# Optimization experiments

Measured on AMD Instinct MI355X. Metric: run time of the kernel, lower is better.

The kernel has to match this reference:

```python
import jax, jax.numpy as jnp
import numpy as np

# ViT-Base-ish encoder: 256x256 img, patch 8 -> N=1024 tokens, dim 768, 8 layers
B, C, H, W = 8, 3, 256, 256
P, D, DEPTH, HEADS, DH, MLP = 8, 768, 8, 12, 64, 3072
N = (H // P) * (W // P)
INNER = HEADS * DH  # 768
EPS = 1e-5


def setup_inputs() -> dict:
    key = jax.random.key(0)
    ks = jax.random.split(key, 8)
    s = lambda i, shape, scale=0.02: jax.random.normal(ks[i], shape, jnp.float32) * scale
    return {
        "x": s(0, (B, C, H, W), 1.0),
        "w_conv": s(1, (D, C, P, P)),          # OIHW conv kernel (patch embed)
        "b_conv": jnp.zeros((D,), jnp.float32),
        "pos_emb": s(2, (1, N, D)),
        "ln1_w": jnp.ones((DEPTH, D), jnp.float32),
        "ln1_b": jnp.zeros((DEPTH, D), jnp.float32),
        "qkv_w": s(3, (DEPTH, D, 3 * INNER)),  # stored [in,out]; Linear has no bias
        "out_w": s(4, (DEPTH, INNER, D)),
        "out_b": jnp.zeros((DEPTH, D), jnp.float32),
        "ln2_w": jnp.ones((DEPTH, D), jnp.float32),
        "ln2_b": jnp.zeros((DEPTH, D), jnp.float32),
        "w1": s(5, (DEPTH, D, MLP)),
        "b1": jnp.zeros((DEPTH, MLP), jnp.float32),
        "w2": s(6, (DEPTH, MLP, D)),
        "b2": jnp.zeros((DEPTH, D), jnp.float32),
    }


def _layernorm(x, w, b):
    m = jnp.mean(x, axis=-1, keepdims=True)
    v = jnp.mean(jnp.square(x - m), axis=-1, keepdims=True)
    return (x - m) * jax.lax.rsqrt(v + EPS) * w + b


def _encoder(x, w_conv, b_conv, pos_emb, ln1_w, ln1_b, qkv_w, out_w, out_b,
             ln2_w, ln2_b, w1, b1, w2, b2):
    # PatchEmbed: strided conv -> flatten(2).transpose(1,2)
    h = jax.lax.conv_general_dilated(
        x, w_conv, window_strides=(P, P), padding='VALID',
        dimension_numbers=('NCHW', 'OIHW', 'NCHW'))
    h = h + b_conv[None, :, None, None]
    h = h.reshape(B, D, N).transpose(0, 2, 1)  # [B, N, D]
    h = h + pos_emb
    scale = DH ** -0.5

    def block(h, p):
        l1w, l1b, qkvw, ow, ob, l2w, l2b, W1, B1, W2, B2 = p
        # PreNorm + MHSA
        y = _layernorm(h, l1w, l1b)
        qkv = y @ qkvw                                   # [B,N,3*INNER]
        q, k, v = jnp.split(qkv, 3, axis=-1)
        split_heads = lambda t: t.reshape(B, N, HEADS, DH).transpose(0, 2, 1, 3)
        q, k, v = split_heads(q), split_heads(k), split_heads(v)
        attn = jax.nn.softmax(jnp.einsum('bhnd,bhmd->bhnm', q, k) * scale, axis=-1)
        o = jnp.einsum('bhnm,bhmd->bhnd', attn, v)
        o = o.transpose(0, 2, 1, 3).reshape(B, N, INNER)
        h = h + (o @ ow + ob)
        # PreNorm + FFN (exact GELU, dropout=0)
        y = _layernorm(h, l2w, l2b)
        h = h + (jax.nn.gelu(y @ W1 + B1, approximate=False) @ W2 + B2)
        return h, None

    h, _ = jax.lax.scan(block, h, (ln1_w, ln1_b, qkv_w, out_w, out_b,
                                   ln2_w, ln2_b, w1, b1, w2, b2))
    return h


def reference(x, w_conv, b_conv, pos_emb, ln1_w, ln1_b, qkv_w, out_w, out_b,
              ln2_w, ln2_b, w1, b1, w2, b2):
    return _encoder(x, w_conv, b_conv, pos_emb, ln1_w, ln1_b, qkv_w, out_w,
                    out_b, ln2_w, ln2_b, w1, b1, w2, b2)
```

## Files before the change

kernel.cpp:

```cpp
#include <hip/hip_runtime.h>
#include <math.h>

#define BATCH 8
#define CIN 3
#define HIMG 256
#define WIMG 256
#define PATCH 8
#define DMODEL 768
#define DEPTH 8
#define HEADS 12
#define DHEAD 64
#define MLPDIM 3072
#define NTOK 1024
#define INNER 768
#define MROWS (BATCH * NTOK)
#define QKVS (3 * INNER)
#define KPATCH (CIN * PATCH * PATCH)
#define LNEPS 1e-5f
#define QSCALE 0.18033688011112042f

typedef __attribute__((ext_vector_type(8))) short short8;
typedef __attribute__((ext_vector_type(4))) float v4f;

__device__ __forceinline__ float b2f(unsigned short u) {
  union { unsigned int i; float f; } x;
  x.i = (unsigned int)u << 16;
  return x.f;
}
__device__ __forceinline__ unsigned short f2b(float f) {
  union { float f; unsigned int i; } x;
  x.f = f;
  unsigned int r = x.i + 0x7FFFu + ((x.i >> 16) & 1u);
  return (unsigned short)(r >> 16);
}
__device__ __forceinline__ unsigned int pkrh(float a, float b) {
  union { float f; unsigned int u; } x, y;
  x.f = a; y.f = b;
  return ((x.u + 0x8000u) >> 16) | ((y.u + 0x8000u) & 0xFFFF0000u);
}

#define GLL(gp, lp)                                                     \
  __builtin_amdgcn_global_load_lds(                                     \
      (const __attribute__((address_space(1))) void*)(gp),              \
      (__attribute__((address_space(3))) void*)(lp), 16, 0, 0)

__global__ __launch_bounds__(256) void cast_kernel(
    const float* __restrict__ src, unsigned short* __restrict__ dst, int n) {
  int i = blockIdx.x * 256 + threadIdx.x;
  if (i < n) dst[i] = f2b(src[i]);
}

__global__ __launch_bounds__(256) void transpose_cast_kernel(
    const float* __restrict__ src, unsigned short* __restrict__ dst, int R,
    int C) {
  __shared__ unsigned short t[32][33];
  src += (size_t)blockIdx.z * R * C;
  dst += (size_t)blockIdx.z * R * C;
  int c0 = blockIdx.x * 32, r0 = blockIdx.y * 32;
  int tx = threadIdx.x & 31, ty = threadIdx.x >> 5;
#pragma unroll
  for (int u = 0; u < 4; ++u) {
    int r = r0 + ty + u * 8;
    t[ty + u * 8][tx] = f2b(src[(size_t)r * C + c0 + tx]);
  }
  __syncthreads();
#pragma unroll
  for (int u = 0; u < 4; ++u) {
    int c = c0 + ty + u * 8;
    dst[(size_t)c * R + r0 + tx] = t[tx][ty + u * 8];
  }
}

__global__ __launch_bounds__(256) void vtrans_kernel(
    const unsigned short* __restrict__ qkv, unsigned short* __restrict__ vt) {
  __shared__ unsigned short t[32][33];
  int k0 = blockIdx.x * 32;
  int d0 = blockIdx.y * 32;
  int bh = blockIdx.z;
  int b = bh / HEADS, h = bh % HEADS;
  int tx = threadIdx.x & 31, ty = threadIdx.x >> 5;
  const unsigned short* src =
      qkv + (size_t)(b * NTOK) * QKVS + 2 * INNER + h * DHEAD;
#pragma unroll
  for (int u = 0; u < 4; ++u)
    t[ty + u * 8][tx] = src[(size_t)(k0 + ty + u * 8) * QKVS + d0 + tx];
  __syncthreads();
  unsigned short* dst = vt + ((size_t)bh * DHEAD + d0) * NTOK + k0;
#pragma unroll
  for (int u = 0; u < 4; ++u)
    dst[(size_t)(ty + u * 8) * NTOK + tx] = t[tx][ty + u * 8];
}

__global__ __launch_bounds__(256) void im2col_kernel(
    const float* __restrict__ x, unsigned short* __restrict__ A) {
  int idx = blockIdx.x * 256 + threadIdx.x;
  if (idx >= MROWS * KPATCH) return;
  int m = idx / KPATCH, k = idx % KPATCH;
  int b = m / NTOK, n = m % NTOK;
  int ph = n / 32, pw = n % 32;
  int c = k / 64, r = k % 64;
  int py = r / 8, px = r % 8;
  A[idx] =
      f2b(x[((size_t)(b * CIN + c) * HIMG + ph * 8 + py) * WIMG + pw * 8 + px]);
}

template <int EPI, int OB, int MT>
__global__ __launch_bounds__(256) void mfma_gemm_kernel(
    const unsigned short* __restrict__ Ag, const unsigned short* __restrict__ Bt,
    const float* __restrict__ bias, const float* __restrict__ res,
    void* __restrict__ Cg, int Mdim, int Ndim, int Kdim) {
  constexpr int MI = MT / 32;
  constexpr int RA = MT / 4;
  constexpr int NCA = RA / 8;
  __shared__ __align__(16) unsigned short Asm[MT * 64];
  __shared__ __align__(16) unsigned short Bsm[128 * 64];
  int tid = threadIdx.x;
  int lane = tid & 63, wv = tid >> 6;

  int Nt = Ndim / 128;
  int mchunk = (Mdim / MT) >> 3;
  int bid = blockIdx.x;
  int xcd = bid & 7;
  int j = bid >> 3;
  int m0 = (xcd * mchunk + j / Nt) * MT;
  int n0 = (j % Nt) * 128;

  v4f acc[MI][4] = {};

  int sr8 = lane >> 3;
  int sc8 = ((lane & 7) ^ sr8) * 8;
  const unsigned short* Aw = Ag + (size_t)(m0 + RA * wv + sr8) * Kdim + sc8;
  const unsigned short* Bw = Bt + (size_t)(n0 + 32 * wv + sr8) * Kdim + sc8;
  unsigned short* As0 = Asm + (RA * wv) * 64;
  unsigned short* Bs0 = Bsm + (32 * wv) * 64;

  int quad = lane >> 4, lr = lane & 15;
  int fr0 = (wv >> 1) * (MI * 16);
  int fc0 = (wv & 1) * 64;
  int xcol = (quad ^ (lr & 7)) * 8;
  const unsigned short* Afr = Asm + (fr0 + lr) * 64;
  const unsigned short* Bfr = Bsm + (fc0 + lr) * 64;

  for (int k0 = 0; k0 < Kdim; k0 += 64) {
#pragma unroll
    for (int c = 0; c < NCA; ++c)
      GLL(Aw + k0 + (size_t)(8 * c) * Kdim, As0 + c * 8 * 64);
#pragma unroll
    for (int c = 0; c < 4; ++c)
      GLL(Bw + k0 + (size_t)(8 * c) * Kdim, Bs0 + c * 8 * 64);
    __syncthreads();
#pragma unroll
    for (int s = 0; s < 2; ++s) {
      int xo = xcol ^ (s * 32);
      short8 af[MI], bf[4];
#pragma unroll
      for (int i = 0; i < MI; ++i)
        af[i] = *(const short8*)(Afr + i * 16 * 64 + xo);
#pragma unroll
      for (int n = 0; n < 4; ++n)
        bf[n] = *(const short8*)(Bfr + n * 16 * 64 + xo);
#pragma unroll
      for (int i = 0; i < MI; ++i)
#pragma unroll
        for (int n = 0; n < 4; ++n)
          acc[i][n] = __builtin_amdgcn_mfma_f32_16x16x32_bf16(
              af[i], bf[n], acc[i][n], 0, 0, 0);
    }
    __syncthreads();
  }

  float* Cf = (float*)Cg;
  unsigned short* Cb = (unsigned short*)Cg;
#pragma unroll
  for (int i = 0; i < MI; ++i) {
#pragma unroll
    for (int n = 0; n < 4; ++n) {
      int ncol = n0 + fc0 + 16 * n + lr;
#pragma unroll
      for (int reg = 0; reg < 4; ++reg) {
        int mrow = m0 + fr0 + 16 * i + quad * 4 + reg;
        float v = acc[i][n][reg];
        if (EPI == 2 || EPI == 3 || EPI == 4) v += bias[ncol];
        if (EPI == 2) v += res[(size_t)mrow * Ndim + ncol];
        if (EPI == 3) {
          float u = v * (0.7978845608028654f + 0.035677408136300125f * v * v);
          float a = fminf(fmaxf(u * 2.8853900817779268f, -60.f), 60.f);
          float E = __builtin_amdgcn_exp2f(a);
          v = v * E * __builtin_amdgcn_rcpf(E + 1.0f);
        }
        if (EPI == 4) v += res[(size_t)(mrow % NTOK) * Ndim + ncol];
        if (EPI == 5 && ncol < INNER) v *= QSCALE;
        if (OB)
          Cb[(size_t)mrow * Ndim + ncol] = f2b(v);
        else
          Cf[(size_t)mrow * Ndim + ncol] = v;
      }
    }
  }
}

#define ABUF (256 * 64)
#define BBUF (128 * 64)
#define SM8B ((3 * ABUF + 3 * BBUF) * 2)

template <int EPI, int OB>
__global__ __launch_bounds__(512, 2) void gemm8_kernel(
    const unsigned short* __restrict__ Ag, const unsigned short* __restrict__ Bt,
    const float* __restrict__ bias, const float* __restrict__ res,
    void* __restrict__ Cg, int Mdim, int Ndim, int Kdim) {
  extern __shared__ __align__(16) unsigned short sm8[];
  unsigned short* As = sm8;
  unsigned short* Bs = sm8 + 3 * ABUF;
  int tid = threadIdx.x;
  int lane = tid & 63, wv = tid >> 6;
  int wm = wv >> 1, wn = wv & 1;
  int quad = lane >> 4, lr = lane & 15;

  int Nt = Ndim / 128;
  int mchunk = (Mdim / 256) >> 3;
  int bid = blockIdx.x;
  int xcd = bid & 7;
  int j = bid >> 3;
  int m0 = (xcd * mchunk + j / Nt) * 256;
  int n0 = (j % Nt) * 128;
  int NTI = Kdim >> 6;

  int sr8 = lane >> 3;
  int sc8 = ((lane & 7) ^ sr8) * 8;
  const unsigned short* Aw = Ag + (size_t)(m0 + wv * 8 + sr8) * Kdim + sc8;
  const unsigned short* Bw = Bt + (size_t)(n0 + wv * 8 + sr8) * Kdim + sc8;
  unsigned short* AsW = As + (wv * 8) * 64;
  unsigned short* BsW = Bs + (wv * 8) * 64;

  int xq = (quad ^ (lr & 7)) * 8;
  const unsigned short* Afr = As + (wm * 64 + lr) * 64;
  const unsigned short* Bfr = Bs + (wn * 64 + lr) * 64;

  v4f acc[4][4] = {};

#pragma unroll
  for (int t = 0; t < 2; ++t) {
#pragma unroll
    for (int r = 0; r < 4; ++r)
      GLL(Aw + t * 64 + (size_t)(64 * r) * Kdim, AsW + t * ABUF + r * 64 * 64);
#pragma unroll
    for (int r = 0; r < 2; ++r)
      GLL(Bw + t * 64 + (size_t)(64 * r) * Kdim, BsW + t * BBUF + r * 64 * 64);
  }
  asm volatile("s_waitcnt vmcnt(6)" ::: "memory");
  __builtin_amdgcn_s_barrier();

  int rb = 0, sb = 2;
  for (int t = 0; t < NTI; ++t) {
    const unsigned short* Afb = Afr + rb * ABUF;
    const unsigned short* Bfb = Bfr + rb * BBUF;
    const unsigned short* Ak = Aw + (t + 2) * 64;
    const unsigned short* Bk = Bw + (t + 2) * 64;
    unsigned short* Ad = AsW + sb * ABUF;
    unsigned short* Bd = BsW + sb * BBUF;
    bool st = (t + 2 < NTI);

    short8 af[2][4], bf[2][2];
#pragma unroll
    for (int s2 = 0; s2 < 2; ++s2) {
      int xo = xq ^ (s2 * 32);
#pragma unroll
      for (int m = 0; m < 4; ++m)
        af[s2][m] = *(const short8*)(Afb + m * 16 * 64 + xo);
#pragma unroll
      for (int n = 0; n < 2; ++n)
        bf[s2][n] = *(const short8*)(Bfb + n * 16 * 64 + xo);
    }
    if (st) {
#pragma unroll
      for (int r = 0; r < 3; ++r)
        GLL(Ak + (size_t)(64 * r) * Kdim, Ad + r * 64 * 64);
    }
    __builtin_amdgcn_s_barrier();
    asm volatile("s_waitcnt lgkmcnt(0)" ::: "memory");
    __builtin_amdgcn_sched_barrier(0);
    __builtin_amdgcn_s_setprio(1);
#pragma unroll
    for (int s2 = 0; s2 < 2; ++s2)
#pragma unroll
      for (int m = 0; m < 4; ++m)
#pragma unroll
        for (int n = 0; n < 2; ++n)
          acc[m][n] = __builtin_amdgcn_mfma_f32_16x16x32_bf16(
              af[s2][m], bf[s2][n], acc[m][n], 0, 0, 0);
    __builtin_amdgcn_s_setprio(0);
    __builtin_amdgcn_s_barrier();

    short8 bg[2][2];
#pragma unroll
    for (int s2 = 0; s2 < 2; ++s2) {
      int xo = xq ^ (s2 * 32);
#pragma unroll
      for (int n = 0; n < 2; ++n)
        bg[s2][n] = *(const short8*)(Bfb + (32 + n * 16) * 64 + xo);
    }
    if (st) {
      GLL(Ak + (size_t)(64 * 3) * Kdim, Ad + 3 * 64 * 64);
#pragma unroll
      for (int r = 0; r < 2; ++r)
        GLL(Bk + (size_t)(64 * r) * Kdim, Bd + r * 64 * 64);
    }
    if (t + 2 < NTI) {
      asm volatile("s_waitcnt vmcnt(6)" ::: "memory");
    } else if (t + 1 < NTI) {
      asm volatile("s_waitcnt vmcnt(0)" ::: "memory");
    }
    __builtin_amdgcn_s_barrier();
    asm volatile("s_waitcnt lgkmcnt(0)" ::: "memory");
    __builtin_amdgcn_sched_barrier(0);
    __builtin_amdgcn_s_setprio(1);
#pragma unroll
    for (int s2 = 0; s2 < 2; ++s2)
#pragma unroll
      for (int m = 0; m < 4; ++m)
#pragma unroll
        for (int n = 0; n < 2; ++n)
          acc[m][n + 2] = __builtin_amdgcn_mfma_f32_16x16x32_bf16(
              af[s2][m], bg[s2][n], acc[m][n + 2], 0, 0, 0);
    __builtin_amdgcn_s_setprio(0);
    __builtin_amdgcn_s_barrier();

    rb = (rb == 2) ? 0 : rb + 1;
    sb = (sb == 2) ? 0 : sb + 1;
  }

  float* Cf = (float*)Cg;
  unsigned short* Cb = (unsigned short*)Cg;
#pragma unroll
  for (int i = 0; i < 4; ++i) {
#pragma unroll
    for (int n = 0; n < 4; ++n) {
      int ncol = n0 + wn * 64 + 16 * n + lr;
#pragma unroll
      for (int reg = 0; reg < 4; ++reg) {
        int mrow = m0 + wm * 64 + 16 * i + quad * 4 + reg;
        float v = acc[i][n][reg];
        if (EPI == 2 || EPI == 3) v += bias[ncol];
        if (EPI == 2) v += res[(size_t)mrow * Ndim + ncol];
        if (EPI == 3) {
          float u = v * (0.7978845608028654f + 0.035677408136300125f * v * v);
          float a = fminf(fmaxf(u * 2.8853900817779268f, -60.f), 60.f);
          float E = __builtin_amdgcn_exp2f(a);
          v = v * E * __builtin_amdgcn_rcpf(E + 1.0f);
        }
        if (EPI == 5 && ncol < INNER) v *= QSCALE;
        if (OB)
          Cb[(size_t)mrow * Ndim + ncol] = f2b(v);
        else
          Cf[(size_t)mrow * Ndim + ncol] = v;
      }
    }
  }
}

__global__ __launch_bounds__(256) void ln_kernel(
    const float* __restrict__ x, const float* __restrict__ w,
    const float* __restrict__ b, unsigned short* __restrict__ y) {
  int row = blockIdx.x;
  const float* xr = x + (size_t)row * DMODEL;
  unsigned short* yr = y + (size_t)row * DMODEL;
  int tid = threadIdx.x;
  float v0 = xr[tid], v1 = xr[tid + 256], v2 = xr[tid + 512];
  float s = v0 + v1 + v2;
  __shared__ float red[4];
#pragma unroll
  for (int off = 32; off >= 1; off >>= 1) s += __shfl_xor(s, off, 64);
  if ((tid & 63) == 0) red[tid >> 6] = s;
  __syncthreads();
  float mean = (red[0] + red[1] + red[2] + red[3]) * (1.0f / DMODEL);
  float d0 = v0 - mean, d1 = v1 - mean, d2 = v2 - mean;
  float sq = d0 * d0 + d1 * d1 + d2 * d2;
  __syncthreads();
#pragma unroll
  for (int off = 32; off >= 1; off >>= 1) sq += __shfl_xor(sq, off, 64);
  if ((tid & 63) == 0) red[tid >> 6] = sq;
  __syncthreads();
  float var = (red[0] + red[1] + red[2] + red[3]) * (1.0f / DMODEL);
  float rs = rsqrtf(var + LNEPS);
  yr[tid] = f2b(d0 * rs * w[tid] + b[tid]);
  yr[tid + 256] = f2b(d1 * rs * w[tid + 256] + b[tid + 256]);
  yr[tid + 512] = f2b(d2 * rs * w[tid + 512] + b[tid + 512]);
}

__global__ __launch_bounds__(256) void attn_kernel(
    const unsigned short* __restrict__ qkv,
    const unsigned short* __restrict__ vtg, unsigned short* __restrict__ o) {
  __shared__ __align__(16) unsigned short Ks[64 * 64];
  __shared__ __align__(16) unsigned short Vs[64 * 64];
  __shared__ __align__(16) unsigned short Pl[4][32 * 64];
  int tid = threadIdx.x;
  int lane = tid & 63, wv = tid >> 6;
  int quad = lane >> 4, lr = lane & 15;
  int q0 = blockIdx.x * 128, hh = blockIdx.y, bb = blockIdx.z;

  const unsigned short* qg =
      qkv + (size_t)(bb * NTOK + q0 + wv * 32) * QKVS + hh * DHEAD;
  const unsigned short* kg =
      qkv + (size_t)(bb * NTOK) * QKVS + INNER + hh * DHEAD;
  const unsigned short* vg = vtg + (size_t)(bb * HEADS + hh) * DHEAD * NTOK;
  unsigned short* Pw = Pl[wv];

  int srow = lane >> 3, soff = (lane & 7) * 8;
  int xs = ((lane & 7) ^ srow) * 8;
  int xq = (quad ^ (lr & 7)) * 8;

#pragma unroll
  for (int p = 0; p < 4; ++p) {
    int r = p * 8 + srow;
    *(int4*)(Pw + r * 64 + xs) = *(const int4*)(qg + (size_t)r * QKVS + soff);
  }
  short8 qf[2][2];
#pragma unroll
  for (int n = 0; n < 2; ++n)
#pragma unroll
    for (int s = 0; s < 2; ++s)
      qf[n][s] = *(const short8*)(Pw + (n * 16 + lr) * 64 + (xq ^ (s * 32)));

  v4f oac[2][4] = {};
  float m_i[2] = {-1e30f, -1e30f};
  float l_i[2] = {0.f, 0.f};

  for (int t = 0; t < NTOK / 64; ++t) {
    __syncthreads();
#pragma unroll
    for (int p = 0; p < 2; ++p) {
      int r = wv * 16 + p * 8 + srow;
      *(int4*)(Ks + r * 64 + xs) =
          *(const int4*)(kg + (size_t)(t * 64 + r) * QKVS + soff);
      *(int4*)(Vs + r * 64 + xs) =
          *(const int4*)(vg + (size_t)r * NTOK + t * 64 + soff);
    }
    __syncthreads();

    v4f sac[4][2] = {};
#pragma unroll
    for (int s = 0; s < 2; ++s) {
      short8 kf[4];
#pragma unroll
      for (int mt = 0; mt < 4; ++mt)
        kf[mt] = *(const short8*)(Ks + (mt * 16 + lr) * 64 + (xq ^ (s * 32)));
#pragma unroll
      for (int mt = 0; mt < 4; ++mt)
#pragma unroll
        for (int n = 0; n < 2; ++n)
          sac[mt][n] = __builtin_amdgcn_mfma_f32_16x16x32_bf16(
              kf[mt], qf[n][s], sac[mt][n], 0, 0, 0);
    }

#pragma unroll
    for (int n = 0; n < 2; ++n) {
      float mx = -1e30f;
#pragma unroll
      for (int mt = 0; mt < 4; ++mt)
#pragma unroll
        for (int r = 0; r < 4; ++r) mx = fmaxf(mx, sac[mt][n][r]);
      mx = fmaxf(mx, __shfl_xor(mx, 16, 64));
      mx = fmaxf(mx, __shfl_xor(mx, 32, 64));
      float mnew = fmaxf(m_i[n], mx);
      float alpha = __builtin_amdgcn_exp2f(m_i[n] - mnew);
      m_i[n] = mnew;
      float sum = 0.f;
#pragma unroll
      for (int mt = 0; mt < 4; ++mt) {
#pragma unroll
        for (int r = 0; r < 4; ++r) {
          float p = __builtin_amdgcn_exp2f(sac[mt][n][r] - mnew);
          sac[mt][n][r] = p;
          sum += p;
        }
        *(uint2*)(Pw + (n * 16 + lr) * 64 +
                  (((mt * 2 + (quad >> 1)) ^ (lr & 7)) * 8) + (quad & 1) * 4) =
            make_uint2(pkrh(sac[mt][n][0], sac[mt][n][1]),
                       pkrh(sac[mt][n][2], sac[mt][n][3]));
      }
      sum += __shfl_xor(sum, 16, 64);
      sum += __shfl_xor(sum, 32, 64);
      l_i[n] = l_i[n] * alpha + sum;
#pragma unroll
      for (int r = 0; r < 4; ++r) {
        float ao = __shfl(alpha, quad * 4 + r, 64);
#pragma unroll
        for (int j = 0; j < 4; ++j) oac[n][j][r] *= ao;
      }
    }

#pragma unroll
    for (int s = 0; s < 2; ++s) {
      short8 pf[2], vf[4];
#pragma unroll
      for (int i = 0; i < 2; ++i)
        pf[i] = *(const short8*)(Pw + (i * 16 + lr) * 64 + (xq ^ (s * 32)));
#pragma unroll
      for (int j = 0; j < 4; ++j)
        vf[j] = *(const short8*)(Vs + (j * 16 + lr) * 64 + (xq ^ (s * 32)));
#pragma unroll
      for (int i = 0; i < 2; ++i)
#pragma unroll
        for (int j = 0; j < 4; ++j)
          oac[i][j] = __builtin_amdgcn_mfma_f32_16x16x32_bf16(
              pf[i], vf[j], oac[i][j], 0, 0, 0);
    }
  }

  unsigned short* ob =
      o + (size_t)(bb * NTOK + q0 + wv * 32) * INNER + hh * DHEAD;
#pragma unroll
  for (int i = 0; i < 2; ++i) {
    float inv = 1.0f / l_i[i];
#pragma unroll
    for (int r = 0; r < 4; ++r) {
      float il = __shfl(inv, quad * 4 + r, 64);
      int row = i * 16 + quad * 4 + r;
#pragma unroll
      for (int j = 0; j < 4; ++j)
        ob[(size_t)row * INNER + 16 * j + lr] = f2b(oac[i][j][r] * il);
    }
  }
}

extern "C" void kernel_launch(void* const* d_in, const int* in_sizes, int n_in,
                              void* d_out, int out_size, void* d_ws,
                              size_t ws_size, hipStream_t stream) {
  const float* x      = (const float*)d_in[0];
  const float* w_conv = (const float*)d_in[1];
  const float* b_conv = (const float*)d_in[2];
  const float* pos    = (const float*)d_in[3];
  const float* ln1w   = (const float*)d_in[4];
  const float* ln1b   = (const float*)d_in[5];
  const float* qkvw   = (const float*)d_in[6];
  const float* outw   = (const float*)d_in[7];
  const float* outb   = (const float*)d_in[8];
  const float* ln2w   = (const float*)d_in[9];
  const float* ln2b   = (const float*)d_in[10];
  const float* w1     = (const float*)d_in[11];
  const float* b1     = (const float*)d_in[12];
  const float* w2     = (const float*)d_in[13];
  const float* b2     = (const float*)d_in[14];

  char* ws = (char*)d_ws;
  float* outp = (float*)d_out;
  dim3 blk(256);
  dim3 blk8(512);

  static bool attr_done = false;
  if (!attr_done) {
    (void)hipFuncSetAttribute(
        reinterpret_cast<const void*>(&gemm8_kernel<5, 1>),
        hipFuncAttributeMaxDynamicSharedMemorySize, SM8B);
    (void)hipFuncSetAttribute(
        reinterpret_cast<const void*>(&gemm8_kernel<2, 0>),
        hipFuncAttributeMaxDynamicSharedMemorySize, SM8B);
    (void)hipFuncSetAttribute(
        reinterpret_cast<const void*>(&gemm8_kernel<3, 1>),
        hipFuncAttributeMaxDynamicSharedMemorySize, SM8B);
    attr_done = true;
  }

  float* h            = (float*)(ws + 0);
  unsigned short* big = (unsigned short*)(ws + 25165824);
  unsigned short* y   = (unsigned short*)(ws + 75497472);

  const size_t NEEDED = 214204416;
  bool batched = ws_size >= NEEDED;

  unsigned short *vt, *wc, *wqa, *woa, *w1a, *w2a;
  unsigned short *wq_f, *wo_f, *w1_f, *w2_f;
  if (batched) {
    vt  = (unsigned short*)(ws + 88080384);
    wc  = (unsigned short*)(ws + 100663296);
    wqa = (unsigned short*)(ws + 100958208);
    woa = (unsigned short*)(ws + 129269760);
    w1a = (unsigned short*)(ws + 138706944);
    w2a = (unsigned short*)(ws + 176455680);
    wq_f = wo_f = w1_f = w2_f = nullptr;
  } else {
    wq_f = (unsigned short*)(ws + 88080384);
    wo_f = (unsigned short*)(ws + 91619328);
    w1_f = (unsigned short*)(ws + 92798976);
    w2_f = (unsigned short*)(ws + 97517568);
    wc   = (unsigned short*)(ws + 102236160);
    vt   = (unsigned short*)(ws + 102531072);
    wqa = woa = w1a = w2a = nullptr;
  }

  cast_kernel<<<dim3((DMODEL * KPATCH + 255) / 256), blk, 0, stream>>>(
      w_conv, wc, DMODEL * KPATCH);
  im2col_kernel<<<dim3((MROWS * KPATCH + 255) / 256), blk, 0, stream>>>(x, big);
  mfma_gemm_kernel<4, 0, 64>
      <<<dim3((MROWS / 64) * (DMODEL / 128)), blk, 0, stream>>>(
          big, wc, b_conv, pos, h, MROWS, DMODEL, KPATCH);

  if (batched) {
    transpose_cast_kernel<<<dim3(QKVS / 32, DMODEL / 32, DEPTH), blk, 0,
                            stream>>>(qkvw, wqa, DMODEL, QKVS);
    transpose_cast_kernel<<<dim3(DMODEL / 32, INNER / 32, DEPTH), blk, 0,
                            stream>>>(outw, woa, INNER, DMODEL);
    transpose_cast_kernel<<<dim3(MLPDIM / 32, DMODEL / 32, DEPTH), blk, 0,
                            stream>>>(w1, w1a, DMODEL, MLPDIM);
    transpose_cast_kernel<<<dim3(DMODEL / 32, MLPDIM / 32, DEPTH), blk, 0,
                            stream>>>(w2, w2a, MLPDIM, DMODEL);
  }

  for (int l = 0; l < DEPTH; ++l) {
    unsigned short* wq = batched ? wqa + (size_t)l * DMODEL * QKVS : wq_f;
    unsigned short* wo = batched ? woa + (size_t)l * INNER * DMODEL : wo_f;
    unsigned short* w1t = batched ? w1a + (size_t)l * DMODEL * MLPDIM : w1_f;
    unsigned short* w2t = batched ? w2a + (size_t)l * MLPDIM * DMODEL : w2_f;
    if (!batched) {
      transpose_cast_kernel<<<dim3(QKVS / 32, DMODEL / 32), blk, 0, stream>>>(
          qkvw + (size_t)l * DMODEL * QKVS, wq, DMODEL, QKVS);
    }
    ln_kernel<<<dim3(MROWS), blk, 0, stream>>>(h, ln1w + l * DMODEL,
                                               ln1b + l * DMODEL, y);
    gemm8_kernel<5, 1>
        <<<dim3((MROWS / 256) * (QKVS / 128)), blk8, SM8B, stream>>>(
            y, wq, nullptr, nullptr, big, MROWS, QKVS, DMODEL);
    vtrans_kernel<<<dim3(NTOK / 32, DHEAD / 32, BATCH * HEADS), blk, 0,
                    stream>>>(big, vt);
    attn_kernel<<<dim3(NTOK / 128, HEADS, BATCH), blk, 0, stream>>>(big, vt, y);
    if (!batched) {
      transpose_cast_kernel<<<dim3(DMODEL / 32, INNER / 32), blk, 0, stream>>>(
          outw + (size_t)l * INNER * DMODEL, wo, INNER, DMODEL);
    }
    gemm8_kernel<2, 0>
        <<<dim3((MROWS / 256) * (DMODEL / 128)), blk8, SM8B, stream>>>(
            y, wo, outb + l * DMODEL, h, h, MROWS, DMODEL, INNER);
    ln_kernel<<<dim3(MROWS), blk, 0, stream>>>(h, ln2w + l * DMODEL,
                                               ln2b + l * DMODEL, y);
    if (!batched) {
      transpose_cast_kernel<<<dim3(MLPDIM / 32, DMODEL / 32), blk, 0, stream>>>(
          w1 + (size_t)l * DMODEL * MLPDIM, w1t, DMODEL, MLPDIM);
    }
    gemm8_kernel<3, 1>
        <<<dim3((MROWS / 256) * (MLPDIM / 128)), blk8, SM8B, stream>>>(
            y, w1t, b1 + l * MLPDIM, nullptr, big, MROWS, MLPDIM, DMODEL);
    if (!batched) {
      transpose_cast_kernel<<<dim3(DMODEL / 32, MLPDIM / 32), blk, 0, stream>>>(
          w2 + (size_t)l * MLPDIM * DMODEL, w2t, MLPDIM, DMODEL);
    }
    float* dst = (l == DEPTH - 1) ? outp : h;
    gemm8_kernel<2, 0>
        <<<dim3((MROWS / 256) * (DMODEL / 128)), blk8, SM8B, stream>>>(
            big, w2t, b2 + l * DMODEL, h, dst, MROWS, DMODEL, MLPDIM);
  }
}
```

Baseline: 2.362 ms.

## Use 256x256 ping-pong GEMM for wide projections and lazy softmax rescale

Replaces the 256x128 triple-buffered GEMM with a 256x256 tile kernel for the QKV and FFN1 projections. It uses double-buffered LDS and an eight-phase interleave of LDS reads, global loads and MFMA blocks. The narrow residual GEMMs (out-projection and FFN2) go back to the smaller mfma_gemm kernel with 64-row tiles, which gives more blocks for N=768. The attention kernel now skips the running-max rescale of the output accumulators unless the new max exceeds the old one by more than 8. This trades a little numeric headroom for fewer exps and shuffles. The larger tile raises register and LDS pressure and leaves fewer blocks for the QKV GEMM.

```diff
diff --git a/kernel.cpp b/kernel.cpp
--- a/kernel.cpp
+++ b/kernel.cpp
@@ -199,30 +199,29 @@
   }
 }
 
-#define ABUF (256 * 64)
-#define BBUF (128 * 64)
-#define SM8B ((3 * ABUF + 3 * BBUF) * 2)
+#define ABUF8 (256 * 64)
+#define BBUF8 (256 * 64)
+#define SM8PH (2 * (ABUF8 + BBUF8) * 2)
 
 template <int EPI, int OB>
-__global__ __launch_bounds__(512, 2) void gemm8_kernel(
+__global__ __launch_bounds__(512, 2) void gemm8ph_kernel(
     const unsigned short* __restrict__ Ag, const unsigned short* __restrict__ Bt,
-    const float* __restrict__ bias, const float* __restrict__ res,
-    void* __restrict__ Cg, int Mdim, int Ndim, int Kdim) {
+    const float* __restrict__ bias, void* __restrict__ Cg, int Mdim, int Ndim,
+    int Kdim) {
   extern __shared__ __align__(16) unsigned short sm8[];
   unsigned short* As = sm8;
-  unsigned short* Bs = sm8 + 3 * ABUF;
+  unsigned short* Bs = sm8 + 2 * ABUF8;
   int tid = threadIdx.x;
   int lane = tid & 63, wv = tid >> 6;
-  int wm = wv >> 1, wn = wv & 1;
+  int wm = wv >> 2, wn = wv & 3;
   int quad = lane >> 4, lr = lane & 15;
 
-  int Nt = Ndim / 128;
-  int mchunk = (Mdim / 256) >> 3;
+  int Nt = Ndim >> 8;
+  int mchunk = (Mdim >> 8) >> 3;
   int bid = blockIdx.x;
-  int xcd = bid & 7;
-  int j = bid >> 3;
-  int m0 = (xcd * mchunk + j / Nt) * 256;
-  int n0 = (j % Nt) * 128;
+  int xcd = bid & 7, j = bid >> 3;
+  int m0 = (xcd * mchunk + j / Nt) << 8;
+  int n0 = (j % Nt) << 8;
   int NTI = Kdim >> 6;
 
   int sr8 = lane >> 3;
@@ -233,116 +232,163 @@
   unsigned short* BsW = Bs + (wv * 8) * 64;
 
   int xq = (quad ^ (lr & 7)) * 8;
-  const unsigned short* Afr = As + (wm * 64 + lr) * 64;
+  const unsigned short* Afr = As + (wm * 128 + lr) * 64;
   const unsigned short* Bfr = Bs + (wn * 64 + lr) * 64;
-
-  v4f acc[4][4] = {};
-
-#pragma unroll
-  for (int t = 0; t < 2; ++t) {
-#pragma unroll
-    for (int r = 0; r < 4; ++r)
-      GLL(Aw + t * 64 + (size_t)(64 * r) * Kdim, AsW + t * ABUF + r * 64 * 64);
-#pragma unroll
-    for (int r = 0; r < 2; ++r)
-      GLL(Bw + t * 64 + (size_t)(64 * r) * Kdim, BsW + t * BBUF + r * 64 * 64);
-  }
-  asm volatile("s_waitcnt vmcnt(6)" ::: "memory");
-  __builtin_amdgcn_s_barrier();
-
-  int rb = 0, sb = 2;
-  for (int t = 0; t < NTI; ++t) {
-    const unsigned short* Afb = Afr + rb * ABUF;
-    const unsigned short* Bfb = Bfr + rb * BBUF;
-    const unsigned short* Ak = Aw + (t + 2) * 64;
-    const unsigned short* Bk = Bw + (t + 2) * 64;
-    unsigned short* Ad = AsW + sb * ABUF;
-    unsigned short* Bd = BsW + sb * BBUF;
-    bool st = (t + 2 < NTI);
-
-    short8 af[2][4], bf[2][2];
-#pragma unroll
-    for (int s2 = 0; s2 < 2; ++s2) {
-      int xo = xq ^ (s2 * 32);
+  const unsigned short* Afr1 = Afr + ABUF8;
+  const unsigned short* Bfr1 = Bfr + BBUF8;
+
+  v4f acc[8][4] = {};
+  short8 af[2][4], bf0[2][2], bf1[2][2];
+
+#define STG_A8(buf, tile, half)                                           \
+  do {                                                                    \
+    GLL(Aw + (size_t)((half) * 128) * Kdim + (tile) * 64,                 \
+        AsW + (buf) * ABUF8 + ((half) * 128) * 64);                       \
+    GLL(Aw + (size_t)((half) * 128 + 64) * Kdim + (tile) * 64,            \
+        AsW + (buf) * ABUF8 + ((half) * 128 + 64) * 64);                  \
+  } while (0)
+#define STG_B8(buf, tile, half)                                           \
+  do {                                                                    \
+    GLL(Bw + (size_t)((half) * 128) * Kdim + (tile) * 64,                 \
+        BsW + (buf) * BBUF8 + ((half) * 128) * 64);                       \
+    GLL(Bw + (size_t)((half) * 128 + 64) * Kdim + (tile) * 64,            \
+        BsW + (buf) * BBUF8 + ((half) * 128 + 64) * 64);                  \
+  } while (0)
+
+  auto rd_af = [&](const unsigned short* base, int mb) {
+#pragma unroll
+    for (int s = 0; s < 2; ++s)
 #pragma unroll
       for (int m = 0; m < 4; ++m)
-        af[s2][m] = *(const short8*)(Afb + m * 16 * 64 + xo);
+        af[s][m] =
+            *(const short8*)(base + (mb + m * 16) * 64 + (xq ^ (s * 32)));
+  };
+  auto rd_bf0 = [&](const unsigned short* base, int nb) {
+#pragma unroll
+    for (int s = 0; s < 2; ++s)
 #pragma unroll
       for (int n = 0; n < 2; ++n)
-        bf[s2][n] = *(const short8*)(Bfb + n * 16 * 64 + xo);
-    }
-    if (st) {
-#pragma unroll
-      for (int r = 0; r < 3; ++r)
-        GLL(Ak + (size_t)(64 * r) * Kdim, Ad + r * 64 * 64);
-    }
+        bf0[s][n] =
+            *(const short8*)(base + (nb + n * 16) * 64 + (xq ^ (s * 32)));
+  };
+  auto rd_bf1 = [&](const unsigned short* base, int nb) {
+#pragma unroll
+    for (int s = 0; s < 2; ++s)
+#pragma unroll
+      for (int n = 0; n < 2; ++n)
+        bf1[s][n] =
+            *(const short8*)(base + (nb + n * 16) * 64 + (xq ^ (s * 32)));
+  };
+  auto mfma0 = [&](int mb, int nb) {
+#pragma unroll
+    for (int s = 0; s < 2; ++s)
+#pragma unroll
+      for (int m = 0; m < 4; ++m)
+#pragma unroll
+        for (int n = 0; n < 2; ++n)
+          acc[mb + m][nb + n] = __builtin_amdgcn_mfma_f32_16x16x32_bf16(
+              af[s][m], bf0[s][n], acc[mb + m][nb + n], 0, 0, 0);
+  };
+  auto mfma1 = [&](int mb, int nb) {
+#pragma unroll
+    for (int s = 0; s < 2; ++s)
+#pragma unroll
+      for (int m = 0; m < 4; ++m)
+#pragma unroll
+        for (int n = 0; n < 2; ++n)
+          acc[mb + m][nb + n] = __builtin_amdgcn_mfma_f32_16x16x32_bf16(
+              af[s][m], bf1[s][n], acc[mb + m][nb + n], 0, 0, 0);
+  };
+  auto mfma_begin = [&]() {
     __builtin_amdgcn_s_barrier();
     asm volatile("s_waitcnt lgkmcnt(0)" ::: "memory");
     __builtin_amdgcn_sched_barrier(0);
     __builtin_amdgcn_s_setprio(1);
-#pragma unroll
-    for (int s2 = 0; s2 < 2; ++s2)
-#pragma unroll
-      for (int m = 0; m < 4; ++m)
-#pragma unroll
-        for (int n = 0; n < 2; ++n)
-          acc[m][n] = __builtin_amdgcn_mfma_f32_16x16x32_bf16(
-              af[s2][m], bf[s2][n], acc[m][n], 0, 0, 0);
+  };
+  auto mfma_end = [&]() {
     __builtin_amdgcn_s_setprio(0);
     __builtin_amdgcn_s_barrier();
-
-    short8 bg[2][2];
-#pragma unroll
-    for (int s2 = 0; s2 < 2; ++s2) {
-      int xo = xq ^ (s2 * 32);
-#pragma unroll
-      for (int n = 0; n < 2; ++n)
-        bg[s2][n] = *(const short8*)(Bfb + (32 + n * 16) * 64 + xo);
-    }
+  };
+
+  STG_B8(0, 0, 0);
+  STG_B8(0, 0, 1);
+  STG_A8(0, 0, 0);
+  STG_A8(0, 0, 1);
+  STG_B8(1, 1, 0);
+  STG_B8(1, 1, 1);
+  asm volatile("s_waitcnt vmcnt(4)" ::: "memory");
+  __builtin_amdgcn_s_barrier();
+
+  int NI = NTI >> 1;
+  for (int i = 0; i < NI; ++i) {
+    int t1 = 2 * i + 1, t2 = 2 * i + 2, t3 = 2 * i + 3;
+    bool st = t2 < NTI;
+
+    rd_af(Afr, 0);
+    rd_bf0(Bfr, 0);
+    STG_A8(1, t1, 0);
+    mfma_begin();
+    mfma0(0, 0);
+    mfma_end();
+    rd_bf1(Bfr, 32);
+    STG_A8(1, t1, 1);
+    mfma_begin();
+    mfma1(0, 2);
+    mfma_end();
+    rd_af(Afr, 64);
+    if (st) STG_B8(0, t2, 0);
+    mfma_begin();
+    mfma0(4, 0);
+    mfma_end();
     if (st) {
-      GLL(Ak + (size_t)(64 * 3) * Kdim, Ad + 3 * 64 * 64);
-#pragma unroll
-      for (int r = 0; r < 2; ++r)
-        GLL(Bk + (size_t)(64 * r) * Kdim, Bd + r * 64 * 64);
-    }
-    if (t + 2 < NTI) {
-      asm volatile("s_waitcnt vmcnt(6)" ::: "memory");
-    } else if (t + 1 < NTI) {
+      STG_B8(0, t2, 1);
+      asm volatile("s_waitcnt vmcnt(4)" ::: "memory");
+    } else {
       asm volatile("s_waitcnt vmcnt(0)" ::: "memory");
     }
-    __builtin_amdgcn_s_barrier();
-    asm volatile("s_waitcnt lgkmcnt(0)" ::: "memory");
-    __builtin_amdgcn_sched_barrier(0);
-    __builtin_amdgcn_s_setprio(1);
-#pragma unroll
-    for (int s2 = 0; s2 < 2; ++s2)
-#pragma unroll
-      for (int m = 0; m < 4; ++m)
-#pragma unroll
-        for (int n = 0; n < 2; ++n)
-          acc[m][n + 2] = __builtin_amdgcn_mfma_f32_16x16x32_bf16(
-              af[s2][m], bg[s2][n], acc[m][n + 2], 0, 0, 0);
-    __builtin_amdgcn_s_setprio(0);
-    __builtin_amdgcn_s_barrier();
-
-    rb = (rb == 2) ? 0 : rb + 1;
-    sb = (sb == 2) ? 0 : sb + 1;
-  }
+    mfma_begin();
+    mfma1(4, 2);
+    mfma_end();
+    rd_af(Afr1, 0);
+    rd_bf0(Bfr1, 0);
+    if (st) STG_A8(0, t2, 0);
+    mfma_begin();
+    mfma0(0, 0);
+    mfma_end();
+    rd_bf1(Bfr1, 32);
+    if (st) STG_A8(0, t2, 1);
+    mfma_begin();
+    mfma1(0, 2);
+    mfma_end();
+    rd_af(Afr1, 64);
+    if (st) STG_B8(1, t3, 0);
+    mfma_begin();
+    mfma0(4, 0);
+    mfma_end();
+    if (st) {
+      STG_B8(1, t3, 1);
+      asm volatile("s_waitcnt vmcnt(4)" ::: "memory");
+    }
+    mfma_begin();
+    mfma1(4, 2);
+    mfma_end();
+  }
+#undef STG_A8
+#undef STG_B8
 
   float* Cf = (float*)Cg;
   unsigned short* Cb = (unsigned short*)Cg;
 #pragma unroll
-  for (int i = 0; i < 4; ++i) {
+  for (int i = 0; i < 8; ++i) {
 #pragma unroll
     for (int n = 0; n < 4; ++n) {
       int ncol = n0 + wn * 64 + 16 * n + lr;
 #pragma unroll
       for (int reg = 0; reg < 4; ++reg) {
-        int mrow = m0 + wm * 64 + 16 * i + quad * 4 + reg;
+        int mrow = m0 + wm * 128 + 16 * i + quad * 4 + reg;
         float v = acc[i][n][reg];
-        if (EPI == 2 || EPI == 3) v += bias[ncol];
-        if (EPI == 2) v += res[(size_t)mrow * Ndim + ncol];
         if (EPI == 3) {
+          v += bias[ncol];
           float u = v * (0.7978845608028654f + 0.035677408136300125f * v * v);
           float a = fminf(fmaxf(u * 2.8853900817779268f, -60.f), 60.f);
           float E = __builtin_amdgcn_exp2f(a);
@@ -461,15 +507,24 @@
         for (int r = 0; r < 4; ++r) mx = fmaxf(mx, sac[mt][n][r]);
       mx = fmaxf(mx, __shfl_xor(mx, 16, 64));
       mx = fmaxf(mx, __shfl_xor(mx, 32, 64));
-      float mnew = fmaxf(m_i[n], mx);
-      float alpha = __builtin_amdgcn_exp2f(m_i[n] - mnew);
-      m_i[n] = mnew;
+      if (!__all(mx - m_i[n] <= 8.0f)) {
+        float mnew = fmaxf(m_i[n], mx);
+        float alpha = __builtin_amdgcn_exp2f(m_i[n] - mnew);
+        m_i[n] = mnew;
+        l_i[n] *= alpha;
+#pragma unroll
+        for (int r = 0; r < 4; ++r) {
+          float ao = __shfl(alpha, quad * 4 + r, 64);
+#pragma unroll
+          for (int j2 = 0; j2 < 4; ++j2) oac[n][j2][r] *= ao;
+        }
+      }
       float sum = 0.f;
 #pragma unroll
       for (int mt = 0; mt < 4; ++mt) {
 #pragma unroll
         for (int r = 0; r < 4; ++r) {
-          float p = __builtin_amdgcn_exp2f(sac[mt][n][r] - mnew);
+          float p = __builtin_amdgcn_exp2f(sac[mt][n][r] - m_i[n]);
           sac[mt][n][r] = p;
           sum += p;
         }
@@ -480,13 +535,7 @@
       }
       sum += __shfl_xor(sum, 16, 64);
       sum += __shfl_xor(sum, 32, 64);
-      l_i[n] = l_i[n] * alpha + sum;
-#pragma unroll
-      for (int r = 0; r < 4; ++r) {
-        float ao = __shfl(alpha, quad * 4 + r, 64);
-#pragma unroll
-        for (int j = 0; j < 4; ++j) oac[n][j][r] *= ao;
-      }
+      l_i[n] += sum;
     }
 
 #pragma unroll
@@ -547,18 +596,15 @@
   dim3 blk(256);
   dim3 blk8(512);
 
-  static bool attr_done = false;
-  if (!attr_done) {
-    (void)hipFuncSetAttribute(
-        reinterpret_cast<const void*>(&gemm8_kernel<5, 1>),
-        hipFuncAttributeMaxDynamicSharedMemorySize, SM8B);
-    (void)hipFuncSetAttribute(
-        reinterpret_cast<const void*>(&gemm8_kernel<2, 0>),
-        hipFuncAttributeMaxDynamicSharedMemorySize, SM8B);
-    (void)hipFuncSetAttribute(
-        reinterpret_cast<const void*>(&gemm8_kernel<3, 1>),
-        hipFuncAttributeMaxDynamicSharedMemorySize, SM8B);
-    attr_done = true;
+  static int use8ph = -1;
+  if (use8ph < 0) {
+    hipError_t e1 = hipFuncSetAttribute(
+        reinterpret_cast<const void*>(&gemm8ph_kernel<5, 1>),
+        hipFuncAttributeMaxDynamicSharedMemorySize, SM8PH);
+    hipError_t e2 = hipFuncSetAttribute(
+        reinterpret_cast<const void*>(&gemm8ph_kernel<3, 1>),
+        hipFuncAttributeMaxDynamicSharedMemorySize, SM8PH);
+    use8ph = (e1 == hipSuccess && e2 == hipSuccess) ? 1 : 0;
   }
 
   float* h            = (float*)(ws + 0);
@@ -617,9 +663,14 @@
     }
     ln_kernel<<<dim3(MROWS), blk, 0, stream>>>(h, ln1w + l * DMODEL,
                                                ln1b + l * DMODEL, y);
-    gemm8_kernel<5, 1>
-        <<<dim3((MROWS / 256) * (QKVS / 128)), blk8, SM8B, stream>>>(
-            y, wq, nullptr, nullptr, big, MROWS, QKVS, DMODEL);
+    if (use8ph)
+      gemm8ph_kernel<5, 1>
+          <<<dim3((MROWS / 256) * (QKVS / 256)), blk8, SM8PH, stream>>>(
+              y, wq, nullptr, big, MROWS, QKVS, DMODEL);
+    else
+      mfma_gemm_kernel<5, 1, 128>
+          <<<dim3((MROWS / 128) * (QKVS / 128)), blk, 0, stream>>>(
+              y, wq, nullptr, nullptr, big, MROWS, QKVS, DMODEL);
     vtrans_kernel<<<dim3(NTOK / 32, DHEAD / 32, BATCH * HEADS), blk, 0,
                     stream>>>(big, vt);
     attn_kernel<<<dim3(NTOK / 128, HEADS, BATCH), blk, 0, stream>>>(big, vt, y);
@@ -627,8 +678,8 @@
       transpose_cast_kernel<<<dim3(DMODEL / 32, INNER / 32), blk, 0, stream>>>(
           outw + (size_t)l * INNER * DMODEL, wo, INNER, DMODEL);
     }
-    gemm8_kernel<2, 0>
-        <<<dim3((MROWS / 256) * (DMODEL / 128)), blk8, SM8B, stream>>>(
+    mfma_gemm_kernel<2, 0, 64>
+        <<<dim3((MROWS / 64) * (DMODEL / 128)), blk, 0, stream>>>(
             y, wo, outb + l * DMODEL, h, h, MROWS, DMODEL, INNER);
     ln_kernel<<<dim3(MROWS), blk, 0, stream>>>(h, ln2w + l * DMODEL,
                                                ln2b + l * DMODEL, y);
@@ -636,16 +687,21 @@
       transpose_cast_kernel<<<dim3(MLPDIM / 32, DMODEL / 32), blk, 0, stream>>>(
           w1 + (size_t)l * DMODEL * MLPDIM, w1t, DMODEL, MLPDIM);
     }
-    gemm8_kernel<3, 1>
-        <<<dim3((MROWS / 256) * (MLPDIM / 128)), blk8, SM8B, stream>>>(
-            y, w1t, b1 + l * MLPDIM, nullptr, big, MROWS, MLPDIM, DMODEL);
+    if (use8ph)
+      gemm8ph_kernel<3, 1>
+          <<<dim3((MROWS / 256) * (MLPDIM / 256)), blk8, SM8PH, stream>>>(
+              y, w1t, b1 + l * MLPDIM, big, MROWS, MLPDIM, DMODEL);
+    else
+      mfma_gemm_kernel<3, 1, 128>
+          <<<dim3((MROWS / 128) * (MLPDIM / 128)), blk, 0, stream>>>(
+              y, w1t, b1 + l * MLPDIM, nullptr, big, MROWS, MLPDIM, DMODEL);
     if (!batched) {
       transpose_cast_kernel<<<dim3(DMODEL / 32, MLPDIM / 32), blk, 0, stream>>>(
           w2 + (size_t)l * MLPDIM * DMODEL, w2t, MLPDIM, DMODEL);
     }
     float* dst = (l == DEPTH - 1) ? outp : h;
-    gemm8_kernel<2, 0>
-        <<<dim3((MROWS / 256) * (DMODEL / 128)), blk8, SM8B, stream>>>(
+    mfma_gemm_kernel<2, 0, 64>
+        <<<dim3((MROWS / 64) * (DMODEL / 128)), blk, 0, stream>>>(
             big, w2t, b2 + l * DMODEL, h, dst, MROWS, DMODEL, MLPDIM);
   }
 }
```

New measurement: 2.326 ms. No clear change (-1.5%).
